# Optimization experiments

Hardware: AMD Instinct MI355X
Metric: run time of the kernel (lower is better)

The kernel has to match this reference:

```python
import jax, jax.numpy as jnp
import numpy as np

N_CLASSES = 3
FEAT_SIZES = (64, 32)  # source1 64x64, source2 32x32 for 512x512 input


def conv(x, w, b):
    # x: NCHW, w: OIHW, 3x3 SAME, stride 1
    y = jax.lax.conv_general_dilated(
        x, w, window_strides=(1, 1), padding='SAME',
        dimension_numbers=('NCHW', 'OIHW', 'NCHW'))
    return y + b[None, :, None, None]


def maxpool(x):
    return jax.lax.reduce_window(x, -jnp.inf, jax.lax.max,
                                 (1, 1, 2, 2), (1, 1, 2, 2), 'VALID')


def l2norm(x, gamma, eps=1e-10):
    # standard SSD L2Norm: per-position channel L2 normalize, learned per-channel scale
    n = jnp.sqrt(jnp.sum(x * x, axis=1, keepdims=True)) + eps
    return gamma[None, :, None, None] * x / n


def make_priors():
    # PriorBox: one prior per feature-map cell, normalized (cx, cy) centers
    ps = []
    for f in FEAT_SIZES:
        c = (jnp.arange(f, dtype=jnp.float32) + 0.5) / f
        cy, cx = jnp.meshgrid(c, c, indexing='ij')
        ps.append(jnp.stack([cx.ravel(), cy.ravel()], axis=1))  # [f*f, 2]
    return jnp.concatenate(ps, axis=0)  # [5120, 2]


def setup_inputs() -> dict:
    key = jax.random.key(0)
    ks = iter(jax.random.split(key, 32))

    def he(k, shape):
        fan_in = shape[1] * shape[2] * shape[3]
        return jax.random.normal(k, shape, jnp.float32) * (2.0 / fan_in) ** 0.5

    d = {'x': jax.random.normal(next(ks), (8, 2, 512, 512), jnp.float32)}
    shapes = [(64, 2, 3, 3), (64, 64, 3, 3), (128, 64, 3, 3), (128, 128, 3, 3),
              (256, 128, 3, 3), (256, 256, 3, 3), (256, 256, 3, 3), (256, 256, 3, 3)]
    for n, s in enumerate(shapes, 1):
        d[f'w{n}'] = he(next(ks), s)
        d[f'b{n}'] = jnp.zeros((s[0],), jnp.float32)
    d['g1'] = 20.0 * jnp.ones((256,), jnp.float32)  # L2Norm1 weight
    d['g2'] = 20.0 * jnp.ones((256,), jnp.float32)  # L2Norm2 weight
    for pre, oc in (('l', 2), ('c', N_CLASSES), ('r', 1)):
        for si in (1, 2):
            d[f'{pre}w{si}'] = he(next(ks), (oc, 256, 3, 3))
            d[f'{pre}b{si}'] = jnp.zeros((oc,), jnp.float32)
    return d


def reference(x, w1, b1, w2, b2, w3, b3, w4, b4, w5, b5, w6, b6, w7, b7, w8, b8,
              g1, g2, lw1, lb1, lw2, lb2, cw1, cb1, cw2, cb2, rw1, rb1, rw2, rb2):
    B = x.shape[0]
    r = jax.nn.relu
    # vgg[0:33]
    x = r(conv(x, w1, b1)); x = r(conv(x, w2, b2)); x = maxpool(x)
    x = r(conv(x, w3, b3)); x = r(conv(x, w4, b4)); x = maxpool(x)
    x = r(conv(x, w5, b5)); x = r(conv(x, w6, b6)); x = maxpool(x)
    s1 = l2norm(x, g1)                 # [B,256,64,64]
    # vgg[33:]
    x = maxpool(x)
    x = r(conv(x, w7, b7)); x = r(conv(x, w8, b8))
    s2 = l2norm(x, g2)                 # [B,256,32,32]

    def head(s, w_, b_):
        # conv -> permute(0,2,3,1) -> flatten, as in the torch forward
        return conv(s, w_, b_).transpose(0, 2, 3, 1).reshape(B, -1)

    loc = jnp.concatenate([head(s1, lw1, lb1), head(s2, lw2, lb2)], 1).reshape(B, -1, 2)
    conf = jnp.concatenate([head(s1, cw1, cb1), head(s2, cw2, cb2)], 1).reshape(B, -1, N_CLASSES)
    regr = jnp.concatenate([head(s1, rw1, rb1), head(s2, rw2, rb2)], 1).reshape(B, -1, 1)
    priors = make_priors()
    return loc, conf, regr, priors
```

## Files before the change

### kernel.cpp

```cpp
#include <hip/hip_runtime.h>

typedef _Float16 f16;
typedef _Float16 f16x8 __attribute__((ext_vector_type(8)));
typedef float f32x4 __attribute__((ext_vector_type(4)));

__device__ __forceinline__ f32x4 mfma16(f16x8 a, f16x8 b, f32x4 c) {
    return __builtin_amdgcn_mfma_f32_16x16x32_f16(a, b, c, 0, 0, 0);
}

template<int IC, int OC, int BX, int WY, int WO, int MT, int NT, bool POOL>
__global__ __launch_bounds__(256) void convmf_k(
    const f16* __restrict__ in, const f16* __restrict__ wt,
    const float* __restrict__ bias, f16* __restrict__ out,
    int H, int W, int ocBlocks, long inStride, long outStride)
{
    constexpr int WROWS = MT * 16 / BX;
    constexpr int BROWS = WROWS * WY;
    constexpr int SR = BROWS + 2;
    constexpr int SC = BX + 2;
    constexpr int LOG = (BX == 64) ? 6 : 5;
    constexpr int NPIX = SR * SC;
    constexpr int NISS = (NPIX + 63) / 64;
    constexpr int NPpad = NISS * 64;
    static_assert(WY * WO == 4, "4 waves: wave wv stages part wv");
    static_assert(!POOL || (BX == 64 && MT == 8), "pool path assumes BX==64, MT==8");
    __shared__ f16 lds[4 * NPpad * 8];

    const int tid  = threadIdx.x;
    const int lane = tid & 63;
    const int wv   = tid >> 6;
    const int wy   = wv / WO;
    const int wo   = wv % WO;
    const int lm   = lane & 15;
    const int lk   = lane >> 4;
    const int x0   = blockIdx.x * BX;
    const int y0   = blockIdx.y * BROWS;
    const int zb   = blockIdx.z;
    const int n    = zb / ocBlocks;
    const int oc0  = (zb - n * ocBlocks) * (16 * NT * WO) + wo * (16 * NT);
    in  += (long)n * inStride;
    out += (long)n * outStride;

    f32x4 acc[MT][NT];
#pragma unroll
    for (int mt = 0; mt < MT; ++mt)
#pragma unroll
        for (int nt = 0; nt < NT; ++nt)
            acc[mt][nt] = (f32x4){0.f, 0.f, 0.f, 0.f};

    const int Wp = W + 2;
    for (int ic0 = 0; ic0 < IC; ic0 += 32) {
        if (ic0) __syncthreads();
        const f16* ip = in + ((long)y0 * Wp + x0) * IC + ic0 + wv * 8;
#pragma unroll
        for (int i = 0; i < NISS; ++i) {
            int p = i * 64 + lane;
            int pc = (p < NPIX) ? p : 0;
            int r = pc / SC, xcol = pc - r * SC;
            long off = ((long)r * Wp + xcol) * IC;
            __builtin_amdgcn_global_load_lds(
                (const __attribute__((address_space(1))) void*)(ip + off),
                (__attribute__((address_space(3))) void*)&lds[(long)(wv * NPpad + i * 64) * 8],
                16, 0, 0);
        }
        asm volatile("s_waitcnt vmcnt(0)" ::: "memory");
        __syncthreads();

        for (int t = 0; t < 9; ++t) {
            int dy = t / 3, dx = t - dy * 3;
            const f16* wp = wt + ((long)t * OC + oc0) * IC + ic0 + lk * 8;
            f16x8 bfr[NT];
#pragma unroll
            for (int nt = 0; nt < NT; ++nt)
                bfr[nt] = *(const f16x8*)(wp + (nt * 16 + lm) * IC);
#pragma unroll
            for (int mt = 0; mt < MT; ++mt) {
                int pos = mt * 16 + lm;
                int xx = pos & (BX - 1);
                int yy = wy * WROWS + (pos >> LOG);
                int pp = (yy + dy) * SC + xx + dx;
                f16x8 a = *(const f16x8*)&lds[(lk * NPpad + pp) * 8];
#pragma unroll
                for (int nt = 0; nt < NT; ++nt)
                    acc[mt][nt] = mfma16(a, bfr[nt], acc[mt][nt]);
            }
        }
    }

    if constexpr (!POOL) {
#pragma unroll
        for (int nt = 0; nt < NT; ++nt) {
            int oc = oc0 + nt * 16 + lm;
            float bs = bias[oc];
#pragma unroll
            for (int mt = 0; mt < MT; ++mt) {
#pragma unroll
                for (int r = 0; r < 4; ++r) {
                    int pos = mt * 16 + lk * 4 + r;
                    int xx = pos & (BX - 1);
                    int yy = wy * WROWS + (pos >> LOG);
                    float v = fmaxf(acc[mt][nt][r] + bs, 0.f);
                    out[((long)(y0 + yy + 1) * (W + 2) + (x0 + xx + 1)) * OC + oc] = (f16)v;
                }
            }
        }
    } else {
        const int Wo = W >> 1;
#pragma unroll
        for (int nt = 0; nt < NT; ++nt) {
            int oc = oc0 + nt * 16 + lm;
            float bs = bias[oc];
#pragma unroll
            for (int mt = 0; mt < 4; ++mt) {
#pragma unroll
                for (int r = 0; r < 4; r += 2) {
                    float v = fmaxf(fmaxf(acc[mt][nt][r], acc[mt][nt][r + 1]),
                                    fmaxf(acc[mt + 4][nt][r], acc[mt + 4][nt][r + 1]));
                    v = fmaxf(v + bs, 0.f);
                    int pos = mt * 16 + lk * 4 + r;
                    int xo = pos >> 1;
                    out[((long)((y0 >> 1) + wy + 1) * (Wo + 2) + ((x0 >> 1) + xo + 1)) * OC + oc] = (f16)v;
                }
            }
        }
    }
}

__global__ __launch_bounds__(256) void convmf1_k(
    const float* __restrict__ x, int itemBase,
    const f16* __restrict__ wt1,
    const float* __restrict__ bias, f16* __restrict__ out, long outStride)
{
    __shared__ f16 ldsx[10 * 66 * 2];
    __shared__ f16 ldsa[512 * 40];
    const int tid = threadIdx.x;
    const int lane = tid & 63;
    const int wv = tid >> 6;
    const int lm = lane & 15;
    const int lk = lane >> 4;
    const int x0 = blockIdx.x * 64;
    const int y0 = blockIdx.y * 8;
    const float* xb = x + (long)(itemBase + blockIdx.z) * 2 * 512 * 512;
    out += (long)blockIdx.z * outStride;

    for (int s = tid; s < 660; s += 256) {
        int r = s / 66, xc = s - r * 66;
        int gy = y0 + r - 1, gx = x0 + xc - 1;
        f16 v0 = (f16)0.f, v1 = (f16)0.f;
        if ((unsigned)gy < 512u && (unsigned)gx < 512u) {
            v0 = (f16)xb[(long)gy * 512 + gx];
            v1 = (f16)xb[262144 + (long)gy * 512 + gx];
        }
        ldsx[(r * 66 + xc) * 2]     = v0;
        ldsx[(r * 66 + xc) * 2 + 1] = v1;
    }
    __syncthreads();
    for (int s = tid; s < 2048; s += 256) {
        int pos = s >> 2, g = s & 3;
        int row = pos >> 6, col = pos & 63;
        f16x8 v;
#pragma unroll
        for (int j = 0; j < 8; ++j) {
            int k = g * 8 + j;
            f16 val = (f16)0.f;
            if (k < 18) {
                int t = k >> 1, ic = k & 1;
                int dy = t / 3, dx = t - dy * 3;
                val = ldsx[((row + dy) * 66 + col + dx) * 2 + ic];
            }
            v[j] = val;
        }
        *(f16x8*)&ldsa[pos * 40 + g * 8] = v;
    }
    __syncthreads();

    f32x4 acc[8][4];
#pragma unroll
    for (int mt = 0; mt < 8; ++mt)
#pragma unroll
        for (int nt = 0; nt < 4; ++nt)
            acc[mt][nt] = (f32x4){0.f, 0.f, 0.f, 0.f};

    f16x8 b0 = *(const f16x8*)(wt1 + (0 * 16 + lm) * 32 + lk * 8);
    f16x8 b1 = *(const f16x8*)(wt1 + (1 * 16 + lm) * 32 + lk * 8);
    f16x8 b2 = *(const f16x8*)(wt1 + (2 * 16 + lm) * 32 + lk * 8);
    f16x8 b3 = *(const f16x8*)(wt1 + (3 * 16 + lm) * 32 + lk * 8);
#pragma unroll
    for (int mt = 0; mt < 8; ++mt) {
        int pos = wv * 128 + mt * 16 + lm;
        f16x8 a = *(const f16x8*)&ldsa[pos * 40 + lk * 8];
        acc[mt][0] = mfma16(a, b0, acc[mt][0]);
        acc[mt][1] = mfma16(a, b1, acc[mt][1]);
        acc[mt][2] = mfma16(a, b2, acc[mt][2]);
        acc[mt][3] = mfma16(a, b3, acc[mt][3]);
    }
#pragma unroll
    for (int nt = 0; nt < 4; ++nt) {
        int oc = nt * 16 + lm;
        float bs = bias[oc];
#pragma unroll
        for (int mt = 0; mt < 8; ++mt) {
#pragma unroll
            for (int r = 0; r < 4; ++r) {
                int pos = wv * 128 + mt * 16 + lk * 4 + r;
                int xx = pos & 63, yy = pos >> 6;
                float v = fmaxf(acc[mt][nt][r] + bs, 0.f);
                out[((long)(y0 + yy + 1) * 514 + (x0 + xx + 1)) * 64 + oc] = (f16)v;
            }
        }
    }
}

template<int BX>
__global__ __launch_bounds__(256) void headconv_k(
    const f16* __restrict__ s, long sStride, const f16* __restrict__ wth,
    const float* __restrict__ lb, const float* __restrict__ cb, const float* __restrict__ rb,
    float* __restrict__ loc, float* __restrict__ conf, float* __restrict__ regr,
    int W, int posoff)
{
    constexpr int BY = (BX == 64) ? 1 : 2;
    constexpr int SR = BY + 2, SC = BX + 2;
    constexpr int LOG = (BX == 64) ? 6 : 5;
    __shared__ f16 lds[SR * SC * 40];
    const int tid = threadIdx.x;
    const int lane = tid & 63;
    const int wv = tid >> 6;
    const int lm = lane & 15;
    const int lk = lane >> 4;
    const int y0 = blockIdx.y * BY;
    const int b = blockIdx.z;
    s += (long)b * sStride;

    f32x4 acc = (f32x4){0.f, 0.f, 0.f, 0.f};
    const int Wp = W + 2;
    for (int ic0 = 0; ic0 < 256; ic0 += 32) {
        if (ic0) __syncthreads();
        const f16* ip = s + (long)y0 * Wp * 256 + ic0;
        constexpr int TASKS = SR * SC * 4;
        for (int t = tid; t < TASKS; t += 256) {
            int r = t / (SC * 4);
            int rem = t - r * (SC * 4);
            int xcol = rem >> 2, g = rem & 3;
            f16x8 v = *(const f16x8*)(ip + ((long)r * Wp + xcol) * 256 + g * 8);
            *(f16x8*)&lds[(r * SC + xcol) * 40 + g * 8] = v;
        }
        __syncthreads();
        for (int t = 0; t < 9; ++t) {
            int dy = t / 3, dx = t - dy * 3;
            f16x8 bf = *(const f16x8*)(wth + ((long)t * 16 + lm) * 256 + ic0 + lk * 8);
            int pos = wv * 16 + lm;
            int xx = pos & (BX - 1), yy = pos >> LOG;
            f16x8 a = *(const f16x8*)&lds[((yy + dy) * SC + xx + dx) * 40 + lk * 8];
            acc = mfma16(a, bf, acc);
        }
    }
#pragma unroll
    for (int r = 0; r < 4; ++r) {
        int pos = wv * 16 + lk * 4 + r;
        int xx = pos & (BX - 1), yy = pos >> LOG;
        int P = posoff + (y0 + yy) * W + xx;
        float v = acc[r];
        if (lm < 2)       loc[((long)b * 5120 + P) * 2 + lm]       = v + lb[lm];
        else if (lm < 5)  conf[((long)b * 5120 + P) * 3 + (lm - 2)] = v + cb[lm - 2];
        else if (lm == 5) regr[(long)b * 5120 + P]                  = v + rb[0];
    }
}

__global__ __launch_bounds__(256) void cvt_wt_k(const float* __restrict__ w, f16* __restrict__ wt,
                                                int OC, int IC)
{
    int idx = blockIdx.x * 256 + threadIdx.x;
    if (idx >= OC * IC) return;
    int oc = idx / IC, ic = idx - oc * IC;
#pragma unroll
    for (int t = 0; t < 9; ++t)
        wt[((long)t * OC + oc) * IC + ic] = (f16)w[(long)idx * 9 + t];
}

__global__ __launch_bounds__(64) void cvt_wt1_k(const float* __restrict__ w, f16* __restrict__ wt1)
{
    int oc = threadIdx.x;
#pragma unroll
    for (int k = 0; k < 32; ++k) {
        f16 v = (f16)0.f;
        if (k < 18) {
            int t = k >> 1, ic = k & 1;
            v = (f16)w[((long)oc * 2 + ic) * 9 + t];
        }
        wt1[oc * 32 + k] = v;
    }
}

__global__ __launch_bounds__(256) void cvt_wth_k(const float* __restrict__ lw, const float* __restrict__ cw,
                                                 const float* __restrict__ rw, f16* __restrict__ wth)
{
    int idx = blockIdx.x * 256 + threadIdx.x;
    if (idx >= 9 * 16 * 256) return;
    int t = idx / (16 * 256);
    int r = (idx / 256) & 15;
    int ic = idx & 255;
    float v = 0.f;
    if (r < 2)      v = lw[((long)r * 256 + ic) * 9 + t];
    else if (r < 5) v = cw[((long)(r - 2) * 256 + ic) * 9 + t];
    else if (r == 5) v = rw[(long)ic * 9 + t];
    wth[((long)t * 16 + r) * 256 + ic] = (f16)v;
}

__global__ __launch_bounds__(256) void halo_k(f16* __restrict__ buf, int W, int H, int C,
                                              long stride, int items)
{
    int per = (2 * (W + 2) + 2 * H) * C;
    long total = (long)per * items;
    long idx = (long)blockIdx.x * 256 + threadIdx.x;
    if (idx >= total) return;
    int n = idx / per;
    int j = idx - (long)n * per;
    int c = j % C, p = j / C;
    int row, col;
    if (p < W + 2) { row = 0; col = p; }
    else if (p < 2 * (W + 2)) { row = H + 1; col = p - (W + 2); }
    else { int q = p - 2 * (W + 2); row = 1 + (q >> 1); col = (q & 1) ? (W + 1) : 0; }
    buf[(long)n * stride + ((long)row * (W + 2) + col) * C + c] = (f16)0.f;
}

__global__ __launch_bounds__(256) void l2n_k(const f16* __restrict__ in, const float* __restrict__ g,
                                             f16* __restrict__ out, int W, long stride, int total)
{
    int i = blockIdx.x * 256 + threadIdx.x;
    if (i >= total) return;
    int b = i / (W * W);
    int rem = i - b * W * W;
    int y = rem / W, x = rem - y * W;
    long off = (long)b * stride + ((long)(y + 1) * (W + 2) + x + 1) * 256;
    const f16* p = in + off;
    f16* q = out + off;
    float s = 0.f;
    for (int gg = 0; gg < 32; ++gg) {
        f16x8 v = *(const f16x8*)(p + gg * 8);
#pragma unroll
        for (int j = 0; j < 8; ++j) { float f = (float)v[j]; s = fmaf(f, f, s); }
    }
    float inv = 1.f / (sqrtf(s) + 1e-10f);
    for (int gg = 0; gg < 32; ++gg) {
        f16x8 v = *(const f16x8*)(p + gg * 8);
        f16x8 o;
#pragma unroll
        for (int j = 0; j < 8; ++j) o[j] = (f16)(g[gg * 8 + j] * ((float)v[j] * inv));
        *(f16x8*)(q + gg * 8) = o;
    }
}

__global__ __launch_bounds__(256) void mp_k(const f16* __restrict__ in, f16* __restrict__ out)
{
    int idx = blockIdx.x * 256 + threadIdx.x;
    if (idx >= 8 * 32 * 32 * 32) return;
    int gg = idx & 31;
    int xo = (idx >> 5) & 31;
    int yo = (idx >> 10) & 31;
    int b = idx >> 15;
    const f16* p = in + (long)b * 1115136 + ((long)(2 * yo + 1) * 66 + 2 * xo + 1) * 256 + gg * 8;
    f16x8 a0 = *(const f16x8*)p;
    f16x8 a1 = *(const f16x8*)(p + 256);
    f16x8 a2 = *(const f16x8*)(p + 66 * 256);
    f16x8 a3 = *(const f16x8*)(p + 66 * 256 + 256);
    f16x8 o;
#pragma unroll
    for (int j = 0; j < 8; ++j)
        o[j] = (f16)fmaxf(fmaxf((float)a0[j], (float)a1[j]), fmaxf((float)a2[j], (float)a3[j]));
    *(f16x8*)(out + (long)b * 295936 + ((long)(yo + 1) * 34 + xo + 1) * 256 + gg * 8) = o;
}

__global__ __launch_bounds__(256) void priors_k(float* __restrict__ out)
{
    int r = blockIdx.x * 256 + threadIdx.x;
    if (r >= 5120) return;
    float cx, cy;
    if (r < 4096) {
        int i = r >> 6, j = r & 63;
        cx = (j + 0.5f) / 64.0f; cy = (i + 0.5f) / 64.0f;
    } else {
        int rr = r - 4096;
        int i = rr >> 5, j = rr & 31;
        cx = (j + 0.5f) / 32.0f; cy = (i + 0.5f) / 32.0f;
    }
    out[2 * r] = cx;
    out[2 * r + 1] = cy;
}

extern "C" void kernel_launch(void* const* d_in, const int* in_sizes, int n_in,
                              void* d_out, int out_size, void* d_ws, size_t ws_size,
                              hipStream_t stream)
{
    const float* x  = (const float*)d_in[0];
    const float* w1 = (const float*)d_in[1];  const float* b1 = (const float*)d_in[2];
    const float* w2 = (const float*)d_in[3];  const float* b2 = (const float*)d_in[4];
    const float* w3 = (const float*)d_in[5];  const float* b3 = (const float*)d_in[6];
    const float* w4 = (const float*)d_in[7];  const float* b4 = (const float*)d_in[8];
    const float* w5 = (const float*)d_in[9];  const float* b5 = (const float*)d_in[10];
    const float* w6 = (const float*)d_in[11]; const float* b6 = (const float*)d_in[12];
    const float* w7 = (const float*)d_in[13]; const float* b7 = (const float*)d_in[14];
    const float* w8 = (const float*)d_in[15]; const float* b8 = (const float*)d_in[16];
    const float* g1 = (const float*)d_in[17]; const float* g2 = (const float*)d_in[18];
    const float* lw1 = (const float*)d_in[19]; const float* lb1 = (const float*)d_in[20];
    const float* lw2 = (const float*)d_in[21]; const float* lb2 = (const float*)d_in[22];
    const float* cw1 = (const float*)d_in[23]; const float* cb1 = (const float*)d_in[24];
    const float* cw2 = (const float*)d_in[25]; const float* cb2 = (const float*)d_in[26];
    const float* rw1 = (const float*)d_in[27]; const float* rb1 = (const float*)d_in[28];
    const float* rw2 = (const float*)d_in[29]; const float* rb2 = (const float*)d_in[30];

    f16* wsh = (f16*)d_ws;
    f16* wt2  = wsh + 0;
    f16* wt3  = wsh + 36864;
    f16* wt4  = wsh + 110592;
    f16* wt5  = wsh + 258048;
    f16* wt6  = wsh + 552960;
    f16* wt7  = wsh + 1142784;
    f16* wt8  = wsh + 1732608;
    f16* wt1  = wsh + 2322432;
    f16* wth1 = wsh + 2324480;
    f16* wth2 = wsh + 2361344;
    f16* x6p  = wsh + 2398208;
    const long PI = 11319296;

    const long A1S = 16908544;
    const long P1S = 4260096;
    const long A3S = 8520192;
    const long P2S = 2163200;
    const long A5S = 4326400;
    const long PH2 = 18391040;

    int G = 1;
    for (int g = 8; g >= 1; g >>= 1) {
        long ext = (long)g * (A1S + P1S); if (ext < PH2) ext = PH2;
        if (2.0 * (double)(PI + ext) <= (double)ws_size) { G = g; break; }
    }
    const int NGRP = 8 / G;

    f16* a1 = wsh + PI;
    f16* p1 = wsh + PI + (long)G * A1S;
    f16* a3 = a1;
    f16* p2 = p1;
    f16* a5 = a1;
    f16* s1 = wsh + PI;
    f16* p4 = wsh + PI + 8921088;
    f16* a7 = wsh + PI + 11288576;
    f16* a8 = wsh + PI + 13656064;
    f16* s2 = wsh + PI + 16023552;

    float* loc  = (float*)d_out;
    float* conf = loc + 81920;
    float* regr = loc + 204800;
    float* pri  = loc + 245760;

    cvt_wt_k<<<dim3((64 * 64 + 255) / 256), 256, 0, stream>>>(w2, wt2, 64, 64);
    cvt_wt_k<<<dim3((128 * 64 + 255) / 256), 256, 0, stream>>>(w3, wt3, 128, 64);
    cvt_wt_k<<<dim3((128 * 128 + 255) / 256), 256, 0, stream>>>(w4, wt4, 128, 128);
    cvt_wt_k<<<dim3((256 * 128 + 255) / 256), 256, 0, stream>>>(w5, wt5, 256, 128);
    cvt_wt_k<<<dim3((256 * 256 + 255) / 256), 256, 0, stream>>>(w6, wt6, 256, 256);
    cvt_wt_k<<<dim3((256 * 256 + 255) / 256), 256, 0, stream>>>(w7, wt7, 256, 256);
    cvt_wt_k<<<dim3((256 * 256 + 255) / 256), 256, 0, stream>>>(w8, wt8, 256, 256);
    cvt_wt1_k<<<dim3(1), 64, 0, stream>>>(w1, wt1);
    cvt_wth_k<<<dim3(144), 256, 0, stream>>>(lw1, cw1, rw1, wth1);
    cvt_wth_k<<<dim3(144), 256, 0, stream>>>(lw2, cw2, rw2, wth2);

    for (int grp = 0; grp < NGRP; ++grp) {
        f16* x6g = x6p + (long)grp * G * 1115136;
        halo_k<<<dim3((G * (2 * 514 + 2 * 512) * 64 + 255) / 256), 256, 0, stream>>>(a1, 512, 512, 64, A1S, G);
        halo_k<<<dim3((G * (2 * 258 + 2 * 256) * 64 + 255) / 256), 256, 0, stream>>>(p1, 256, 256, 64, P1S, G);
        convmf1_k<<<dim3(8, 64, G), 256, 0, stream>>>(x, grp * G, wt1, b1, a1, A1S);
        convmf_k<64, 64, 64, 2, 2, 8, 2, true><<<dim3(8, 128, G), 256, 0, stream>>>(
            a1, wt2, b2, p1, 512, 512, 1, A1S, P1S);
        halo_k<<<dim3((G * (2 * 258 + 2 * 256) * 128 + 255) / 256), 256, 0, stream>>>(a3, 256, 256, 128, A3S, G);
        convmf_k<64, 128, 64, 2, 2, 8, 2, false><<<dim3(4, 64, 2 * G), 256, 0, stream>>>(
            p1, wt3, b3, a3, 256, 256, 2, P1S, A3S);
        halo_k<<<dim3((G * (2 * 130 + 2 * 128) * 128 + 255) / 256), 256, 0, stream>>>(p2, 128, 128, 128, P2S, G);
        convmf_k<128, 128, 64, 2, 2, 8, 2, true><<<dim3(4, 64, 2 * G), 256, 0, stream>>>(
            a3, wt4, b4, p2, 256, 256, 2, A3S, P2S);
        halo_k<<<dim3((G * (2 * 130 + 2 * 128) * 256 + 255) / 256), 256, 0, stream>>>(a5, 128, 128, 256, A5S, G);
        convmf_k<128, 256, 64, 2, 2, 8, 2, false><<<dim3(2, 32, 4 * G), 256, 0, stream>>>(
            p2, wt5, b5, a5, 128, 128, 4, P2S, A5S);
        convmf_k<256, 256, 64, 2, 2, 8, 2, true><<<dim3(2, 32, 4 * G), 256, 0, stream>>>(
            a5, wt6, b6, x6g, 128, 128, 4, A5S, 1115136);
    }

    halo_k<<<dim3((8 * (2 * 66 + 2 * 64) * 256 + 255) / 256), 256, 0, stream>>>(s1, 64, 64, 256, 1115136, 8);
    halo_k<<<dim3((8 * (2 * 34 + 2 * 32) * 256 + 255) / 256), 256, 0, stream>>>(p4, 32, 32, 256, 295936, 8);
    halo_k<<<dim3((8 * (2 * 34 + 2 * 32) * 256 + 255) / 256), 256, 0, stream>>>(a7, 32, 32, 256, 295936, 8);
    halo_k<<<dim3((8 * (2 * 34 + 2 * 32) * 256 + 255) / 256), 256, 0, stream>>>(s2, 32, 32, 256, 295936, 8);

    l2n_k<<<dim3((32768 + 255) / 256), 256, 0, stream>>>(x6p, g1, s1, 64, 1115136, 32768);
    mp_k<<<dim3((262144 + 255) / 256), 256, 0, stream>>>(x6p, p4);
    convmf_k<256, 256, 32, 2, 2, 4, 4, false><<<dim3(1, 8, 16), 256, 0, stream>>>(
        p4, wt7, b7, a7, 32, 32, 2, 295936, 295936);
    convmf_k<256, 256, 32, 2, 2, 4, 4, false><<<dim3(1, 8, 16), 256, 0, stream>>>(
        a7, wt8, b8, a8, 32, 32, 2, 295936, 295936);
    l2n_k<<<dim3((8192 + 255) / 256), 256, 0, stream>>>(a8, g2, s2, 32, 295936, 8192);

    headconv_k<64><<<dim3(1, 64, 8), 256, 0, stream>>>(
        s1, 1115136, wth1, lb1, cb1, rb1, loc, conf, regr, 64, 0);
    headconv_k<32><<<dim3(1, 16, 8), 256, 0, stream>>>(
        s2, 295936, wth2, lb2, cb2, rb2, loc, conf, regr, 32, 4096);
    priors_k<<<dim3(20), 256, 0, stream>>>(pri);

    (void)in_sizes; (void)n_in; (void)out_size; (void)ws_size;
}
```

Before: 1.180 ms.

## Double-buffer conv input staging in LDS and allow 8-wave blocks

```diff
diff --git a/kernel.cpp b/kernel.cpp
--- a/kernel.cpp
+++ b/kernel.cpp
@@ -8,29 +8,40 @@
     return __builtin_amdgcn_mfma_f32_16x16x32_f16(a, b, c, 0, 0, 0);
 }
 
+template<int N>
+__device__ __forceinline__ void waitcnt_vm() {
+    asm volatile("s_waitcnt vmcnt(%0)" :: "i"(N) : "memory");
+}
+
 template<int IC, int OC, int BX, int WY, int WO, int MT, int NT, bool POOL>
-__global__ __launch_bounds__(256) void convmf_k(
+__global__ __launch_bounds__(WY * WO * 64) void convmf_k(
     const f16* __restrict__ in, const f16* __restrict__ wt,
     const float* __restrict__ bias, f16* __restrict__ out,
     int H, int W, int ocBlocks, long inStride, long outStride)
 {
+    constexpr int WAVES = WY * WO;
+    constexpr int HALVES = WAVES / 4;
     constexpr int WROWS = MT * 16 / BX;
     constexpr int BROWS = WROWS * WY;
     constexpr int SR = BROWS + 2;
     constexpr int SC = BX + 2;
     constexpr int LOG = (BX == 64) ? 6 : 5;
     constexpr int NPIX = SR * SC;
-    constexpr int NISS = (NPIX + 63) / 64;
-    constexpr int NPpad = NISS * 64;
-    static_assert(WY * WO == 4, "4 waves: wave wv stages part wv");
+    constexpr int STRD = 64 * HALVES;
+    constexpr int NISS = (NPIX + STRD - 1) / STRD;
+    constexpr int NPpad = NISS * STRD;
+    constexpr int NC = IC / 32;
+    static_assert(WAVES == 4 || WAVES == 8, "4 or 8 waves");
     static_assert(!POOL || (BX == 64 && MT == 8), "pool path assumes BX==64, MT==8");
-    __shared__ f16 lds[4 * NPpad * 8];
+    __shared__ f16 lds[2 * 4 * NPpad * 8];
 
     const int tid  = threadIdx.x;
     const int lane = tid & 63;
     const int wv   = tid >> 6;
     const int wy   = wv / WO;
     const int wo   = wv % WO;
+    const int part = wv & 3;
+    const int half = wv >> 2;
     const int lm   = lane & 15;
     const int lk   = lane >> 4;
     const int x0   = blockIdx.x * BX;
@@ -41,6 +52,23 @@
     in  += (long)n * inStride;
     out += (long)n * outStride;
 
+    const int Wp = W + 2;
+    const f16* ipBase = in + ((long)y0 * Wp + x0) * IC + part * 8;
+
+    auto STAGE = [&](int ch, int bi) {
+        const f16* ip = ipBase + ch * 32;
+#pragma unroll
+        for (int i = 0; i < NISS; ++i) {
+            int p = i * STRD + half * 64 + lane;
+            int pc = (p < NPIX) ? p : 0;
+            int r = pc / SC, xcol = pc - r * SC;
+            __builtin_amdgcn_global_load_lds(
+                (const __attribute__((address_space(1))) void*)(ip + ((long)r * Wp + xcol) * IC),
+                (__attribute__((address_space(3))) void*)&lds[((bi * 4 + part) * NPpad + i * STRD + half * 64) * 8],
+                16, 0, 0);
+        }
+    };
+
     f32x4 acc[MT][NT];
 #pragma unroll
     for (int mt = 0; mt < MT; ++mt)
@@ -48,24 +76,19 @@
         for (int nt = 0; nt < NT; ++nt)
             acc[mt][nt] = (f32x4){0.f, 0.f, 0.f, 0.f};
 
-    const int Wp = W + 2;
-    for (int ic0 = 0; ic0 < IC; ic0 += 32) {
-        if (ic0) __syncthreads();
-        const f16* ip = in + ((long)y0 * Wp + x0) * IC + ic0 + wv * 8;
-#pragma unroll
-        for (int i = 0; i < NISS; ++i) {
-            int p = i * 64 + lane;
-            int pc = (p < NPIX) ? p : 0;
-            int r = pc / SC, xcol = pc - r * SC;
-            long off = ((long)r * Wp + xcol) * IC;
-            __builtin_amdgcn_global_load_lds(
-                (const __attribute__((address_space(1))) void*)(ip + off),
-                (__attribute__((address_space(3))) void*)&lds[(long)(wv * NPpad + i * 64) * 8],
-                16, 0, 0);
-        }
-        asm volatile("s_waitcnt vmcnt(0)" ::: "memory");
+    STAGE(0, 0);
+#pragma unroll
+    for (int c = 0; c < NC; ++c) {
+        const int cur = c & 1;
+        if (c + 1 < NC) {
+            STAGE(c + 1, cur ^ 1);
+            waitcnt_vm<NISS>();
+        } else {
+            waitcnt_vm<0>();
+        }
         __syncthreads();
 
+        const int ic0 = c * 32;
         for (int t = 0; t < 9; ++t) {
             int dy = t / 3, dx = t - dy * 3;
             const f16* wp = wt + ((long)t * OC + oc0) * IC + ic0 + lk * 8;
@@ -79,12 +102,13 @@
                 int xx = pos & (BX - 1);
                 int yy = wy * WROWS + (pos >> LOG);
                 int pp = (yy + dy) * SC + xx + dx;
-                f16x8 a = *(const f16x8*)&lds[(lk * NPpad + pp) * 8];
+                f16x8 a = *(const f16x8*)&lds[((cur * 4 + lk) * NPpad + pp) * 8];
 #pragma unroll
                 for (int nt = 0; nt < NT; ++nt)
                     acc[mt][nt] = mfma16(a, bfr[nt], acc[mt][nt]);
             }
         }
+        __syncthreads();
     }
 
     if constexpr (!POOL) {
@@ -468,18 +492,18 @@
         halo_k<<<dim3((G * (2 * 514 + 2 * 512) * 64 + 255) / 256), 256, 0, stream>>>(a1, 512, 512, 64, A1S, G);
         halo_k<<<dim3((G * (2 * 258 + 2 * 256) * 64 + 255) / 256), 256, 0, stream>>>(p1, 256, 256, 64, P1S, G);
         convmf1_k<<<dim3(8, 64, G), 256, 0, stream>>>(x, grp * G, wt1, b1, a1, A1S);
-        convmf_k<64, 64, 64, 2, 2, 8, 2, true><<<dim3(8, 128, G), 256, 0, stream>>>(
+        convmf_k<64, 64, 64, 2, 4, 8, 1, true><<<dim3(8, 128, G), 512, 0, stream>>>(
             a1, wt2, b2, p1, 512, 512, 1, A1S, P1S);
         halo_k<<<dim3((G * (2 * 258 + 2 * 256) * 128 + 255) / 256), 256, 0, stream>>>(a3, 256, 256, 128, A3S, G);
-        convmf_k<64, 128, 64, 2, 2, 8, 2, false><<<dim3(4, 64, 2 * G), 256, 0, stream>>>(
-            p1, wt3, b3, a3, 256, 256, 2, P1S, A3S);
+        convmf_k<64, 128, 64, 2, 4, 8, 2, false><<<dim3(4, 64, G), 512, 0, stream>>>(
+            p1, wt3, b3, a3, 256, 256, 1, P1S, A3S);
         halo_k<<<dim3((G * (2 * 130 + 2 * 128) * 128 + 255) / 256), 256, 0, stream>>>(p2, 128, 128, 128, P2S, G);
-        convmf_k<128, 128, 64, 2, 2, 8, 2, true><<<dim3(4, 64, 2 * G), 256, 0, stream>>>(
-            a3, wt4, b4, p2, 256, 256, 2, A3S, P2S);
+        convmf_k<128, 128, 64, 2, 4, 8, 2, true><<<dim3(4, 64, G), 512, 0, stream>>>(
+            a3, wt4, b4, p2, 256, 256, 1, A3S, P2S);
         halo_k<<<dim3((G * (2 * 130 + 2 * 128) * 256 + 255) / 256), 256, 0, stream>>>(a5, 128, 128, 256, A5S, G);
-        convmf_k<128, 256, 64, 2, 2, 8, 2, false><<<dim3(2, 32, 4 * G), 256, 0, stream>>>(
+        convmf_k<128, 256, 64, 2, 4, 8, 1, false><<<dim3(2, 32, 4 * G), 512, 0, stream>>>(
             p2, wt5, b5, a5, 128, 128, 4, P2S, A5S);
-        convmf_k<256, 256, 64, 2, 2, 8, 2, true><<<dim3(2, 32, 4 * G), 256, 0, stream>>>(
+        convmf_k<256, 256, 64, 2, 4, 8, 1, true><<<dim3(2, 32, 4 * G), 512, 0, stream>>>(
             a5, wt6, b6, x6g, 128, 128, 4, A5S, 1115136);
     }
 
```

New measurement: 1.187 ms. Within noise of the previous version (+0.6%).
